# Kernel optimization log

Measured on AMD Instinct MI355X. Metric: run time of the kernel, lower is better.

The kernel has to match this reference:

```python
import jax, jax.numpy as jnp
import numpy as np

EPS_NORM = 1e-12
EPS_POS = 1e-05
MARGIN = 0.5


def l2_norm(x):
    # matches torch: x / sqrt(sum(x^2, axis=1) + 1e-12)
    norm = jnp.sqrt(jnp.sum(x * x, axis=1) + EPS_NORM)
    return x / norm[:, None]


def setup_inputs() -> dict:
    key = jax.random.key(0)
    k1, k2, k3, k4 = jax.random.split(key, 4)
    n, d, n_classes = 8192, 1024, 1024
    inputs_col = jax.random.normal(k1, (n, d), dtype=jnp.float32)
    inputs_row = jax.random.normal(k2, (n, d), dtype=jnp.float32)
    targets_col = jax.random.randint(k3, (n,), 0, n_classes)
    target_row = jax.random.randint(k4, (n,), 0, n_classes)
    return {"inputs_col": inputs_col, "targets_col": targets_col,
            "inputs_row": inputs_row, "target_row": target_row}


def reference(inputs_col, targets_col, inputs_row, target_row):
    n = inputs_col.shape[0]
    # [n, n] cosine similarity matrix
    sim = l2_norm(inputs_col) @ l2_norm(inputs_row).T
    same = targets_col[:, None] == target_row[None, :]  # [n, n] bool
    pos_mask = same & (sim < 1.0 - EPS_POS)
    neg_mask = (~same) & (sim > MARGIN)
    pos_loss = jnp.sum(jnp.where(pos_mask, 1.0 - sim, 0.0), axis=1)  # [n]
    neg_loss = jnp.sum(jnp.where(neg_mask, sim, 0.0), axis=1)        # [n]
    has_pos = jnp.any(pos_mask, axis=1)  # rows without valid positives are skipped
    row_loss = jnp.where(has_pos, pos_loss + neg_loss, 0.0)
    return jnp.sum(row_loss) / n
```

## Files before the change

### kernel.cpp

```cpp
#include <hip/hip_runtime.h>


constexpr int N = 8192;
constexpr int D = 1024;
constexpr int NT = D / 64;

typedef short bf16x8 __attribute__((ext_vector_type(8)));
typedef float f32x4 __attribute__((ext_vector_type(4)));

static __device__ inline unsigned short f2bf(float f) {
  unsigned int u = __float_as_uint(f);
  unsigned int r = (u + 0x7fffu + ((u >> 16) & 1u)) >> 16;
  return (unsigned short)r;
}

__global__ __launch_bounds__(256) void normalize_kernel(
    const float* __restrict__ in_col, const float* __restrict__ in_row,
    unsigned short* __restrict__ out_col, unsigned short* __restrict__ out_row) {
  int row = blockIdx.x;
  const float* in;
  unsigned short* out;
  if (row < N) {
    in = in_col + (size_t)row * D;
    out = out_col + (size_t)row * D;
  } else {
    in = in_row + (size_t)(row - N) * D;
    out = out_row + (size_t)(row - N) * D;
  }
  int tid = threadIdx.x;
  float4 v = ((const float4*)in)[tid];
  float s = v.x * v.x + v.y * v.y + v.z * v.z + v.w * v.w;
#pragma unroll
  for (int off = 32; off >= 1; off >>= 1) s += __shfl_xor(s, off, 64);
  __shared__ float wsum[4];
  int lane = tid & 63, wid = tid >> 6;
  if (lane == 0) wsum[wid] = s;
  __syncthreads();
  float tot = wsum[0] + wsum[1] + wsum[2] + wsum[3];
  float inv = 1.0f / sqrtf(tot + 1e-12f);
  ushort4 o;
  o.x = f2bf(v.x * inv);
  o.y = f2bf(v.y * inv);
  o.z = f2bf(v.z * inv);
  o.w = f2bf(v.w * inv);
  ((ushort4*)out)[tid] = o;
}

__global__ __launch_bounds__(512, 2) void loss_kernel(
    const unsigned short* __restrict__ An, const unsigned short* __restrict__ Bn,
    const int* __restrict__ tc, const int* __restrict__ tr,
    float* __restrict__ lossG, int* __restrict__ hasG) {
  __shared__ unsigned short lds[65536];

  const int tid = threadIdx.x;
  const int lane = tid & 63;
  const int wid = tid >> 6;
  const int wr = wid >> 2;
  const int wc = wid & 3;

  const int bid = blockIdx.x;
  const int x = bid & 7, s = bid >> 3;
  const int iBase = (((s & 7) | ((s >> 5) << 3))) * 256;
  const int jBase = (x * 4 + ((s >> 3) & 3)) * 256;

  const int frow = lane & 15;
  const int fkb = (lane >> 4) * 16;
  const int rxor = (lane & 7) << 4;
  const int kx0 = (0 + fkb) ^ rxor;
  const int kx1 = (64 + fkb) ^ rxor;
  int rowA[4], rowB[2];
#pragma unroll
  for (int m2 = 0; m2 < 4; m2++) rowA[m2] = (wr * 64 + m2 * 16 + frow) * 128;
#pragma unroll
  for (int n2 = 0; n2 < 2; n2++) rowB[n2] = (wc * 32 + n2 * 16 + frow) * 128;

  const int rl0 = tid >> 3;
  const int kel = (tid & 7) * 8;
  const int kSw = kel ^ ((rl0 & 7) << 3);
  const int rA0 = iBase + rl0;
  const int rB0 = jBase + ((rl0 >> 5) * 64) + (rl0 & 31);

#define GLDS(g, l)                                                        \
  __builtin_amdgcn_global_load_lds(                                       \
      (const __attribute__((address_space(1))) void*)(g),                 \
      (__attribute__((address_space(3))) void*)(l), 16, 0, 0)

#define STAGE_A(h, tt, P)                                                     \
  do {                                                                        \
    const int _k = ((tt) & 15) * 64 + kSw;                                    \
    unsigned short* _d = lds + (((P) * 2 + (h)) * 8192) + wid * 512;          \
    GLDS(An + (size_t)(rA0 + (h) * 64) * D + _k, _d);                         \
    GLDS(An + (size_t)(rA0 + 128 + (h) * 64) * D + _k, _d + 4096);            \
  } while (0)
#define STAGE_B(h, tt, P)                                                     \
  do {                                                                        \
    const int _k = ((tt) & 15) * 64 + kSw;                                    \
    unsigned short* _d = lds + 32768 + (((P) * 2 + (h)) * 8192) + wid * 512;  \
    GLDS(Bn + (size_t)(rB0 + (h) * 32) * D + _k, _d);                         \
    GLDS(Bn + (size_t)(rB0 + 128 + (h) * 32) * D + _k, _d + 4096);            \
  } while (0)

  f32x4 acc[8][4];
#pragma unroll
  for (int mi = 0; mi < 8; mi++)
#pragma unroll
    for (int ni = 0; ni < 4; ni++) acc[mi][ni] = (f32x4){0.f, 0.f, 0.f, 0.f};

  bf16x8 af[4][2], bf[2][2];
  const char* ldsc = (const char*)lds;

  STAGE_A(0, 0, 0);
  STAGE_B(0, 0, 0);
  STAGE_B(1, 0, 0);
  STAGE_A(1, 0, 0);
  STAGE_A(1, 1, 1);
  asm volatile("s_waitcnt vmcnt(2)" ::: "memory");
  __builtin_amdgcn_s_barrier();

#define PH(MIH, NIH, LOADA, LOADB, DA, DB, STG, DRN)                            \
  do {                                                                          \
    if (LOADA) {                                                                \
      _Pragma("unroll") for (int m2 = 0; m2 < 4; m2++) {                        \
        af[m2][0] = *(const bf16x8*)(ldsc + (DA) + (MIH) * 16384 + rowA[m2] + kx0); \
        af[m2][1] = *(const bf16x8*)(ldsc + (DA) + (MIH) * 16384 + rowA[m2] + kx1); \
      }                                                                         \
    }                                                                           \
    if (LOADB) {                                                                \
      _Pragma("unroll") for (int n2 = 0; n2 < 2; n2++) {                        \
        bf[n2][0] = *(const bf16x8*)(ldsc + (DB) + (NIH) * 16384 + rowB[n2] + kx0); \
        bf[n2][1] = *(const bf16x8*)(ldsc + (DB) + (NIH) * 16384 + rowB[n2] + kx1); \
      }                                                                         \
    }                                                                           \
    STG;                                                                        \
    asm volatile("" ::: "memory");                                              \
    __builtin_amdgcn_s_barrier();                                               \
    asm volatile("s_waitcnt lgkmcnt(0)" ::: "memory");                          \
    __builtin_amdgcn_s_setprio(1);                                              \
    _Pragma("unroll") for (int m2 = 0; m2 < 4; m2++)                            \
        _Pragma("unroll") for (int n2 = 0; n2 < 2; n2++)                        \
            _Pragma("unroll") for (int kk = 0; kk < 2; kk++)                    \
                acc[(MIH) * 4 + m2][(NIH) * 2 + n2] =                           \
                    __builtin_amdgcn_mfma_f32_16x16x32_bf16(                    \
                        af[m2][kk], bf[n2][kk],                                 \
                        acc[(MIH) * 4 + m2][(NIH) * 2 + n2], 0, 0, 0);          \
    __builtin_amdgcn_s_setprio(0);                                              \
    DRN;                                                                        \
    asm volatile("" ::: "memory");                                              \
    __builtin_amdgcn_s_barrier();                                               \
  } while (0)

#define DRAIN asm volatile("s_waitcnt vmcnt(2)" ::: "memory")

#define TILE(T, P)                                                              \
  do {                                                                          \
    PH(0, 0, true, true, (P)*32768, 65536 + (P)*32768,                          \
       STAGE_A(0, (T) + 1, 1 - (P)), );                                         \
    PH(0, 1, false, true, (P)*32768, 65536 + (P)*32768,                         \
       STAGE_B(0, (T) + 1, 1 - (P)), );                                         \
    PH(1, 1, true, false, (P)*32768, 65536 + (P)*32768,                         \
       STAGE_B(1, (T) + 1, 1 - (P)), );                                         \
    PH(1, 0, false, true, (P)*32768, 65536 + (P)*32768,                         \
       STAGE_A(1, (T) + 2, (P)), DRAIN);                                        \
  } while (0)

  for (int tp = 0; tp < NT / 2; ++tp) {
    const int t0 = 2 * tp;
    TILE(t0, 0);
    TILE(t0 + 1, 1);
  }
  asm volatile("s_waitcnt vmcnt(0)" ::: "memory");
#undef TILE
#undef PH
#undef DRAIN
#undef STAGE_A
#undef STAGE_B
#undef GLDS

  int trj[4];
#pragma unroll
  for (int ni = 0; ni < 4; ni++) trj[ni] = tr[jBase + wc * 64 + ni * 16 + frow];

#pragma unroll
  for (int mi = 0; mi < 8; mi++) {
#pragma unroll
    for (int r = 0; r < 4; r++) {
      const int i = iBase + wr * 128 + mi * 16 + (lane >> 4) * 4 + r;
      const int tci = tc[i];
      float v = 0.f;
      bool hasp = false;
#pragma unroll
      for (int ni = 0; ni < 4; ni++) {
        float s2 = acc[mi][ni][r];
        if (tci == trj[ni]) {
          if (s2 < 1.0f - 1e-5f) { v += 1.0f - s2; hasp = true; }
        } else if (s2 > 0.5f) {
          v += s2;
        }
      }
#pragma unroll
      for (int off = 1; off < 16; off <<= 1) v += __shfl_xor(v, off, 16);
      unsigned long long m = __ballot(hasp);
      bool rowHas = ((m >> ((lane >> 4) * 16)) & 0xFFFFull) != 0;
      if ((lane & 15) == 0) {
        if (v != 0.f) atomicAdd(&lossG[i], v);
        if (rowHas) atomicOr(&hasG[i], 1);
      }
    }
  }
}

__global__ __launch_bounds__(256) void finalize_kernel(
    const float* __restrict__ lossG, const int* __restrict__ hasG,
    float* __restrict__ out) {
  int tid = threadIdx.x;
  float s = 0.f;
  for (int i = tid; i < N; i += 256)
    if (hasG[i]) s += lossG[i];
#pragma unroll
  for (int off = 32; off >= 1; off >>= 1) s += __shfl_xor(s, off, 64);
  __shared__ float w4[4];
  if ((tid & 63) == 0) w4[tid >> 6] = s;
  __syncthreads();
  if (tid == 0) out[0] = (w4[0] + w4[1] + w4[2] + w4[3]) / (float)N;
}

extern "C" void kernel_launch(void* const* d_in, const int* in_sizes, int n_in,
                              void* d_out, int out_size, void* d_ws, size_t ws_size,
                              hipStream_t stream) {
  const float* in_col = (const float*)d_in[0];
  const int* tcol = (const int*)d_in[1];
  const float* in_row = (const float*)d_in[2];
  const int* trow = (const int*)d_in[3];
  float* out = (float*)d_out;

  char* ws = (char*)d_ws;
  float* lossG = (float*)ws;
  int* hasG = (int*)(ws + (size_t)N * 4);
  unsigned short* colN = (unsigned short*)(ws + (size_t)N * 8);
  unsigned short* rowN = colN + (size_t)N * D;

  hipMemsetAsync(ws, 0, (size_t)N * 8, stream);
  normalize_kernel<<<2 * N, 256, 0, stream>>>(in_col, in_row, colN, rowN);
  loss_kernel<<<1024, 512, 0, stream>>>(colN, rowN, tcol, trow, lossG, hasG);
  finalize_kernel<<<1, 256, 0, stream>>>(lossG, hasG, out);
}
```

Baseline: 297.8 us.

## Halve per-phase barriers in GEMM loop and use one wave per row in normalize

The loss kernel's main loop now has a single barrier per phase instead of two. The needed waits move ahead of the barrier: an LDS-read wait before the third phase and a global-load drain before the fourth. This keeps the buffers safe to overwrite while cutting synchronisation stalls. The MFMA loop is also reordered to put k outermost. The normalize kernel now handles one row per wavefront with only shuffle reductions, removing the LDS round-trip and __syncthreads. The risk is a subtle LDS race if the new wait placement misses a reuse hazard.

```diff
diff --git a/kernel.cpp b/kernel.cpp
--- a/kernel.cpp
+++ b/kernel.cpp
@@ -17,33 +17,31 @@
 __global__ __launch_bounds__(256) void normalize_kernel(
     const float* __restrict__ in_col, const float* __restrict__ in_row,
     unsigned short* __restrict__ out_col, unsigned short* __restrict__ out_row) {
-  int row = blockIdx.x;
-  const float* in;
-  unsigned short* out;
-  if (row < N) {
-    in = in_col + (size_t)row * D;
-    out = out_col + (size_t)row * D;
-  } else {
-    in = in_row + (size_t)(row - N) * D;
-    out = out_row + (size_t)(row - N) * D;
-  }
-  int tid = threadIdx.x;
-  float4 v = ((const float4*)in)[tid];
-  float s = v.x * v.x + v.y * v.y + v.z * v.z + v.w * v.w;
+  int r = blockIdx.x * 4 + (threadIdx.x >> 6);
+  int lane = threadIdx.x & 63;
+  const float* in =
+      (r < N) ? in_col + (size_t)r * D : in_row + (size_t)(r - N) * D;
+  unsigned short* out =
+      (r < N) ? out_col + (size_t)r * D : out_row + (size_t)(r - N) * D;
+  float4 v[4];
+  float s = 0.f;
+#pragma unroll
+  for (int c = 0; c < 4; c++) {
+    v[c] = ((const float4*)in)[lane + c * 64];
+    s += v[c].x * v[c].x + v[c].y * v[c].y + v[c].z * v[c].z + v[c].w * v[c].w;
+  }
 #pragma unroll
   for (int off = 32; off >= 1; off >>= 1) s += __shfl_xor(s, off, 64);
-  __shared__ float wsum[4];
-  int lane = tid & 63, wid = tid >> 6;
-  if (lane == 0) wsum[wid] = s;
-  __syncthreads();
-  float tot = wsum[0] + wsum[1] + wsum[2] + wsum[3];
-  float inv = 1.0f / sqrtf(tot + 1e-12f);
-  ushort4 o;
-  o.x = f2bf(v.x * inv);
-  o.y = f2bf(v.y * inv);
-  o.z = f2bf(v.z * inv);
-  o.w = f2bf(v.w * inv);
-  ((ushort4*)out)[tid] = o;
+  float inv = 1.0f / sqrtf(s + 1e-12f);
+#pragma unroll
+  for (int c = 0; c < 4; c++) {
+    ushort4 o;
+    o.x = f2bf(v[c].x * inv);
+    o.y = f2bf(v[c].y * inv);
+    o.z = f2bf(v[c].z * inv);
+    o.w = f2bf(v[c].w * inv);
+    ((ushort4*)out)[lane + c * 64] = o;
+  }
 }
 
 __global__ __launch_bounds__(512, 2) void loss_kernel(
@@ -116,8 +114,9 @@
   STAGE_A(1, 1, 1);
   asm volatile("s_waitcnt vmcnt(2)" ::: "memory");
   __builtin_amdgcn_s_barrier();
-
-#define PH(MIH, NIH, LOADA, LOADB, DA, DB, STG, DRN)                            \
+  asm volatile("" ::: "memory");
+
+#define PH(MIH, NIH, LOADA, LOADB, DA, DB, STG, PRE)                            \
   do {                                                                          \
     if (LOADA) {                                                                \
       _Pragma("unroll") for (int m2 = 0; m2 < 4; m2++) {                        \
@@ -132,35 +131,32 @@
       }                                                                         \
     }                                                                           \
     STG;                                                                        \
+    if ((PRE) == 1) asm volatile("s_waitcnt lgkmcnt(0)" ::: "memory");          \
+    if ((PRE) == 2) asm volatile("s_waitcnt vmcnt(2)" ::: "memory");            \
     asm volatile("" ::: "memory");                                              \
     __builtin_amdgcn_s_barrier();                                               \
-    asm volatile("s_waitcnt lgkmcnt(0)" ::: "memory");                          \
+    asm volatile("" ::: "memory");                                              \
     __builtin_amdgcn_s_setprio(1);                                              \
-    _Pragma("unroll") for (int m2 = 0; m2 < 4; m2++)                            \
-        _Pragma("unroll") for (int n2 = 0; n2 < 2; n2++)                        \
-            _Pragma("unroll") for (int kk = 0; kk < 2; kk++)                    \
+    _Pragma("unroll") for (int kk = 0; kk < 2; kk++)                            \
+        _Pragma("unroll") for (int m2 = 0; m2 < 4; m2++)                        \
+            _Pragma("unroll") for (int n2 = 0; n2 < 2; n2++)                    \
                 acc[(MIH) * 4 + m2][(NIH) * 2 + n2] =                           \
                     __builtin_amdgcn_mfma_f32_16x16x32_bf16(                    \
                         af[m2][kk], bf[n2][kk],                                 \
                         acc[(MIH) * 4 + m2][(NIH) * 2 + n2], 0, 0, 0);          \
     __builtin_amdgcn_s_setprio(0);                                              \
-    DRN;                                                                        \
-    asm volatile("" ::: "memory");                                              \
-    __builtin_amdgcn_s_barrier();                                               \
-  } while (0)
-
-#define DRAIN asm volatile("s_waitcnt vmcnt(2)" ::: "memory")
+  } while (0)
 
 #define TILE(T, P)                                                              \
   do {                                                                          \
     PH(0, 0, true, true, (P)*32768, 65536 + (P)*32768,                          \
-       STAGE_A(0, (T) + 1, 1 - (P)), );                                         \
+       STAGE_A(0, (T) + 1, 1 - (P)), 0);                                        \
     PH(0, 1, false, true, (P)*32768, 65536 + (P)*32768,                         \
-       STAGE_B(0, (T) + 1, 1 - (P)), );                                         \
+       STAGE_B(0, (T) + 1, 1 - (P)), 0);                                        \
     PH(1, 1, true, false, (P)*32768, 65536 + (P)*32768,                         \
-       STAGE_B(1, (T) + 1, 1 - (P)), );                                         \
+       STAGE_B(1, (T) + 1, 1 - (P)), 1);                                        \
     PH(1, 0, false, true, (P)*32768, 65536 + (P)*32768,                         \
-       STAGE_A(1, (T) + 2, (P)), DRAIN);                                        \
+       STAGE_A(1, (T) + 2, (P)), 2);                                            \
   } while (0)
 
   for (int tp = 0; tp < NT / 2; ++tp) {
@@ -171,7 +167,6 @@
   asm volatile("s_waitcnt vmcnt(0)" ::: "memory");
 #undef TILE
 #undef PH
-#undef DRAIN
 #undef STAGE_A
 #undef STAGE_B
 #undef GLDS
@@ -240,7 +235,7 @@
   unsigned short* rowN = colN + (size_t)N * D;
 
   hipMemsetAsync(ws, 0, (size_t)N * 8, stream);
-  normalize_kernel<<<2 * N, 256, 0, stream>>>(in_col, in_row, colN, rowN);
+  normalize_kernel<<<(2 * N) / 4, 256, 0, stream>>>(in_col, in_row, colN, rowN);
   loss_kernel<<<1024, 512, 0, stream>>>(colN, rowN, tcol, trow, lossG, hasG);
   finalize_kernel<<<1, 256, 0, stream>>>(lossG, hasG, out);
 }
```

Measured after the change: 289.4 us. -2.8%, faster.
